# Kernel tuning notes

Hardware: AMD Instinct MI355X
Metric: run time of the kernel (lower is better)

## Reference

```python
import jax, jax.numpy as jnp
import numpy as np


def _mlp(x, W1, b1, W2, b2, W3, b3):
    # _F: three Linear layers, each followed by ReLU (including the last one)
    x = jax.nn.relu(x @ W1 + b1)
    x = jax.nn.relu(x @ W2 + b2)
    return jax.nn.relu(x @ W3 + b3)


def setup_inputs() -> dict:
    key = jax.random.key(0)
    ks = jax.random.split(key, 11)
    B, L, E, H, O = 2, 4096, 1024, 2048, 3  # batch pinned to 2 by view((2,-1,1))
    std = jnp.float32(0.02)  # small init keeps exp(fa.fb^T) finite in fp32
    z = lambda n: jnp.zeros((n,), jnp.float32)
    return {
        "x1": jax.random.normal(ks[0], (B, L, E), jnp.float32),
        "x2": jax.random.normal(ks[1], (B, L, E), jnp.float32),
        # attend.f = _F(E, H, H)
        "fW1": jax.random.normal(ks[2], (E, H), jnp.float32) * std, "fb1": z(H),
        "fW2": jax.random.normal(ks[3], (H, H), jnp.float32) * std, "fb2": z(H),
        "fW3": jax.random.normal(ks[4], (H, H), jnp.float32) * std, "fb3": z(H),
        # compare.g = _F(E, H, H)
        "gW1": jax.random.normal(ks[5], (E, H), jnp.float32) * std, "gb1": z(H),
        "gW2": jax.random.normal(ks[6], (H, H), jnp.float32) * std, "gb2": z(H),
        "gW3": jax.random.normal(ks[7], (H, H), jnp.float32) * std, "gb3": z(H),
        # aggregate.h = _F(2H, H, O)
        "hW1": jax.random.normal(ks[8], (2 * H, H), jnp.float32) * std, "hb1": z(H),
        "hW2": jax.random.normal(ks[9], (H, H), jnp.float32) * std, "hb2": z(H),
        "hW3": jax.random.normal(ks[10], (H, O), jnp.float32) * std, "hb3": z(O),
    }


def reference(x1, x2,
              fW1, fb1, fW2, fb2, fW3, fb3,
              gW1, gb1, gW2, gb2, gW3, gb3,
              hW1, hb1, hW2, hb2, hW3, hb3):
    # ---- Attend ----
    fa = _mlp(x1, fW1, fb1, fW2, fb2, fW3, fb3)  # (B, L, H)
    fb = _mlp(x2, fW1, fb1, fW2, fb2, fW3, fb3)  # (B, L, H)
    e = jnp.exp(jnp.einsum('bih,bjh->bij', fa, fb))  # (B, L, L), exp-then-normalize as in source
    # beta[b,i] = sum_j (e[b,i,j]/sum_j e[b,i,j]) * x2[b,j]
    beta = jnp.einsum('bij,bje->bie', e / jnp.sum(e, axis=2, keepdims=True), x2)
    # alpha[b,j] = sum_i (e[b,i,j]/sum_i e[b,i,j]) * x1[b,i]
    alpha = jnp.einsum('bij,bie->bje', e / jnp.sum(e, axis=1, keepdims=True), x1)
    # ---- Compare (note: concat along SEQUENCE dim=1, faithful to the source) ----
    v1 = _mlp(jnp.concatenate([x1, beta], axis=1), gW1, gb1, gW2, gb2, gW3, gb3)   # (B, 2L, H)
    v2 = _mlp(jnp.concatenate([x2, alpha], axis=1), gW1, gb1, gW2, gb2, gW3, gb3)  # (B, 2L, H)
    # ---- Aggregate ----
    agg = jnp.concatenate([jnp.sum(v1, axis=1), jnp.sum(v2, axis=1)], axis=1)  # (B, 2H)
    out = _mlp(agg, hW1, hb1, hW2, hb2, hW3, hb3)  # (B, O)
    return out
```

## Files before the change

kernel.cpp:

```cpp
#include <hip/hip_runtime.h>
#include <hip/hip_bf16.h>
#include <cstdint>
#include <cstddef>

typedef unsigned short ushort_t;
typedef __attribute__((ext_vector_type(8))) __bf16 bf16x8;
typedef __attribute__((ext_vector_type(4))) float f32x4;
typedef __attribute__((ext_vector_type(4))) unsigned short us4;

__device__ __forceinline__ unsigned short f2bf(float f) {
    union { __hip_bfloat16 h; unsigned short u; } v;
    v.h = __float2bfloat16(f);
    return v.u;
}
__device__ __forceinline__ float bf2f(unsigned short u) {
    union { unsigned int i; float f; } v;
    v.i = ((unsigned int)u) << 16;
    return v.f;
}

__device__ __forceinline__ void gload16(const void* g, void* l) {
    __builtin_amdgcn_global_load_lds((const __attribute__((address_space(1))) void*)g,
                                     (__attribute__((address_space(3))) void*)l,
                                     16, 0, 0);
}

#define BARRIER() asm volatile("s_barrier" ::: "memory")

template<int EPI>
__global__ __launch_bounds__(512) void gemm256(
        const ushort_t* __restrict__ A, const ushort_t* __restrict__ Bt,
        ushort_t* __restrict__ C, int M, int N, int K,
        const float* __restrict__ epi_vec, float* __restrict__ rowp)
{
    __shared__ __align__(16) ushort_t lds[65536];
    __shared__ float red[2][256];
    __shared__ float rowred[4][256];

    const int nN = N >> 8;
    const int nwg = (int)gridDim.x;
    const int orig = (int)blockIdx.x;
    const int q = nwg >> 3, r = nwg & 7, xcd = orig & 7;
    const int wgid = (xcd < r ? xcd * (q + 1) : r * (q + 1) + (xcd - r) * q) + (orig >> 3);
    const int mb = wgid / nN, nb = wgid % nN;

    const int t = (int)threadIdx.x;
    const int lane = t & 63;
    const int wave = t >> 6;
    const int wm = wave >> 2;
    const int wn = wave & 3;
    const int fr = lane & 15;
    const int fk = lane >> 4;

    const int NT = K >> 6;

    const int l8 = lane >> 3;
    const int lcc = ((lane & 7) ^ (l8 & 7)) * 8;
    const ushort_t* gA = A + (size_t)(mb * 256 + wave * 8 + l8) * (size_t)K + lcc;
    const ushort_t* gB = Bt + (size_t)(nb * 256 + wave * 8 + l8) * (size_t)K + lcc;

    auto stage1 = [&](int op, int dd, int h, int j, int T2) {
        const ushort_t* g = (op ? gB : gA) + (size_t)(h * 128 + j * 64) * (size_t)K + T2 * 64;
        ushort_t* l = lds + ((op * 2 + dd) * 2 + h) * 8192 + j * 4096 + wave * 512;
        gload16(g, l);
    };
    auto stageAB8 = [&](int dd, int T2) {
        stage1(0, dd, 0, 0, T2); stage1(0, dd, 0, 1, T2);
        stage1(0, dd, 1, 0, T2); stage1(0, dd, 1, 1, T2);
        stage1(1, dd, 0, 0, T2); stage1(1, dd, 0, 1, T2);
        stage1(1, dd, 1, 0, T2); stage1(1, dd, 1, 1, T2);
    };

    const int chunk0 = ((fk) ^ (fr & 7)) * 8;
    const int chunk1 = ((4 + fk) ^ (fr & 7)) * 8;

    auto loadA4 = [&](int dd, int kh, int qm, bf16x8* dst) {
        const ushort_t* base = lds + ((0 * 2 + dd) * 2 + wm) * 8192;
        const int ck = kh ? chunk1 : chunk0;
#pragma unroll
        for (int mi = 0; mi < 4; ++mi)
            dst[mi] = *(const bf16x8*)(base + (qm * 64 + mi * 16 + fr) * 64 + ck);
    };
    auto loadB4 = [&](int dd, int kh, bf16x8* dst) {
        const ushort_t* base = lds + ((1 * 2 + dd) * 2 + (wn >> 1)) * 8192;
        const int ck = kh ? chunk1 : chunk0;
#pragma unroll
        for (int ni = 0; ni < 4; ++ni)
            dst[ni] = *(const bf16x8*)(base + ((wn & 1) * 64 + ni * 16 + fr) * 64 + ck);
    };

    f32x4 acc[8][4];
#pragma unroll
    for (int i = 0; i < 8; ++i)
#pragma unroll
        for (int j = 0; j < 4; ++j) acc[i][j] = f32x4{0.f, 0.f, 0.f, 0.f};

#define MM(QM, AV, BV) do {                                                      \
    _Pragma("unroll") for (int mi = 0; mi < 4; ++mi)                             \
    _Pragma("unroll") for (int ni = 0; ni < 4; ++ni)                             \
        acc[(QM) * 4 + mi][ni] = __builtin_amdgcn_mfma_f32_16x16x32_bf16(        \
            AV[mi], BV[ni], acc[(QM) * 4 + mi][ni], 0, 0, 0);                    \
} while (0)

#define TILE_SYNC() do {                                                         \
    __builtin_amdgcn_sched_barrier(0);                                           \
    asm volatile("s_waitcnt lgkmcnt(0) vmcnt(0)" ::: "memory");                  \
    __builtin_amdgcn_sched_barrier(0);                                           \
    BARRIER();                                                                   \
} while (0)

    stageAB8(0, 0);
    asm volatile("s_waitcnt vmcnt(0)" ::: "memory");
    BARRIER();

    for (int T = 0; T < NT; ++T) {
        const int d = T & 1;
        bf16x8 a0[4], a1[4], a2[4], a3[4], b0[4], b1[4];
        loadB4(d, 0, b0);
        loadA4(d, 0, 0, a0);
        if (T + 1 < NT) stageAB8(d ^ 1, T + 1);
        loadA4(d, 0, 1, a1);
        MM(0, a0, b0);
        loadB4(d, 1, b1);
        loadA4(d, 1, 0, a2);
        MM(1, a1, b0);
        loadA4(d, 1, 1, a3);
        MM(0, a2, b1);
        MM(1, a3, b1);
        TILE_SYNC();
    }

#undef MM
#undef TILE_SYNC

    if (EPI == 0) {
#pragma unroll
        for (int mi8 = 0; mi8 < 8; ++mi8) {
            const int row0 = mb * 256 + wm * 128 + (mi8 >> 2) * 64 + (mi8 & 3) * 16 + fk * 4;
#pragma unroll
            for (int ni = 0; ni < 4; ++ni) {
                const int col = nb * 256 + wn * 64 + ni * 16 + fr;
                const float bias = epi_vec[col];
                f32x4 v = acc[mi8][ni];
#pragma unroll
                for (int j = 0; j < 4; ++j)
                    C[(size_t)(row0 + j) * N + col] = f2bf(fmaxf(v[j] + bias, 0.f));
            }
        }
    } else if (EPI == 1) {
        float rsum[8][4];
#pragma unroll
        for (int mi8 = 0; mi8 < 8; ++mi8) {
            const int row0 = mb * 256 + wm * 128 + (mi8 >> 2) * 64 + (mi8 & 3) * 16 + fk * 4;
#pragma unroll
            for (int j = 0; j < 4; ++j) rsum[mi8][j] = 0.f;
#pragma unroll
            for (int ni = 0; ni < 4; ++ni) {
                const int col = nb * 256 + wn * 64 + ni * 16 + fr;
                f32x4 v = acc[mi8][ni];
#pragma unroll
                for (int j = 0; j < 4; ++j) {
                    float x = __expf(v[j]);
                    C[(size_t)(row0 + j) * N + col] = f2bf(x);
                    rsum[mi8][j] += x;
                }
            }
        }
#pragma unroll
        for (int mi8 = 0; mi8 < 8; ++mi8)
#pragma unroll
            for (int j = 0; j < 4; ++j) {
                float s = rsum[mi8][j];
                s += __shfl_xor(s, 1); s += __shfl_xor(s, 2);
                s += __shfl_xor(s, 4); s += __shfl_xor(s, 8);
                rsum[mi8][j] = s;
            }
        if (fr == 0) {
#pragma unroll
            for (int mi8 = 0; mi8 < 8; ++mi8)
#pragma unroll
                for (int j = 0; j < 4; ++j)
                    rowred[wn][wm * 128 + (mi8 >> 2) * 64 + (mi8 & 3) * 16 + fk * 4 + j] = rsum[mi8][j];
        }
        BARRIER();
        if (t < 256)
            rowp[(size_t)nb * M + mb * 256 + t] =
                rowred[0][t] + rowred[1][t] + rowred[2][t] + rowred[3][t];
    } else {
        float cs[4] = {0.f, 0.f, 0.f, 0.f};
#pragma unroll
        for (int ni = 0; ni < 4; ++ni) {
            const int col = nb * 256 + wn * 64 + ni * 16 + fr;
            const float bias = epi_vec[col];
#pragma unroll
            for (int mi8 = 0; mi8 < 8; ++mi8) {
                f32x4 v = acc[mi8][ni];
#pragma unroll
                for (int j = 0; j < 4; ++j) cs[ni] += fmaxf(v[j] + bias, 0.f);
            }
        }
#pragma unroll
        for (int ni = 0; ni < 4; ++ni) {
            float s = cs[ni];
            s += __shfl_down(s, 32);
            s += __shfl_down(s, 16);
            cs[ni] = s;
        }
        if (fk == 0) {
#pragma unroll
            for (int ni = 0; ni < 4; ++ni) red[wm][wn * 64 + ni * 16 + fr] = cs[ni];
        }
        BARRIER();
        if (t < 256) {
            float* colpart = (float*)C;
            colpart[(size_t)mb * N + nb * 256 + t] = red[0][t] + red[1][t];
        }
    }
    asm volatile("s_waitcnt vmcnt(0)" ::: "memory");
}

template<int EPI>
__global__ __launch_bounds__(256) void gemm_bt(
        const ushort_t* __restrict__ A, const ushort_t* __restrict__ Bt,
        ushort_t* __restrict__ C, int M, int N, int K,
        const float* __restrict__ epi_vec)
{
    __shared__ __align__(16) ushort_t As[128 * 32];
    __shared__ __align__(16) ushort_t Bs[128 * 32];

    const int nN = N >> 7;
    const int nwg = (int)gridDim.x;
    const int orig = (int)blockIdx.x;
    const int q = nwg >> 3, r = nwg & 7, xcd = orig & 7;
    const int wgid = (xcd < r ? xcd * (q + 1) : r * (q + 1) + (xcd - r) * q) + (orig >> 3);
    const int mb = wgid / nN, nb = wgid % nN;

    const int t = (int)threadIdx.x;
    const int lane = t & 63;
    const int wave = t >> 6;
    const int wrow = (wave >> 1) << 6;
    const int wcol = (wave & 1) << 6;
    const int fr = lane & 15;
    const int fk = lane >> 4;

    int aoffe[4], boffe[4];
#pragma unroll
    for (int i = 0; i < 4; ++i) {
        int ra = wrow + i * 16 + fr;
        aoffe[i] = ra * 32 + (((fk ^ (ra >> 1)) & 3) << 3);
        int rb = wcol + i * 16 + fr;
        boffe[i] = rb * 32 + (((fk ^ (rb >> 1)) & 3) << 3);
    }

    const int srow = t >> 2;
    const int sslot = (t & 3) ^ ((srow >> 1) & 3);
    const ushort_t* ga = A + (size_t)(mb * 128 + srow) * K + sslot * 8;
    const ushort_t* gb = Bt + (size_t)(nb * 128 + srow) * K + sslot * 8;
    const size_t rowskip = (size_t)64 * K;
    ushort_t* lA0 = As + wave * 512;
    ushort_t* lA1 = As + 2048 + wave * 512;
    ushort_t* lB0 = Bs + wave * 512;
    ushort_t* lB1 = Bs + 2048 + wave * 512;

    f32x4 acc[4][4] = {};

    const int kiters = K >> 5;
    for (int kt = 0; kt < kiters; ++kt) {
        gload16(ga, lA0);
        gload16(ga + rowskip, lA1);
        gload16(gb, lB0);
        gload16(gb + rowskip, lB1);
        __syncthreads();
        bf16x8 af[4], bvv[4];
#pragma unroll
        for (int i = 0; i < 4; ++i) af[i] = *(const bf16x8*)(As + aoffe[i]);
#pragma unroll
        for (int i = 0; i < 4; ++i) bvv[i] = *(const bf16x8*)(Bs + boffe[i]);
#pragma unroll
        for (int mi = 0; mi < 4; ++mi)
#pragma unroll
            for (int ni = 0; ni < 4; ++ni)
                acc[mi][ni] = __builtin_amdgcn_mfma_f32_16x16x32_bf16(af[mi], bvv[ni], acc[mi][ni], 0, 0, 0);
        __syncthreads();
        ga += 32; gb += 32;
    }

#pragma unroll
    for (int mi = 0; mi < 4; ++mi) {
        const int row0 = mb * 128 + wrow + mi * 16 + fk * 4;
#pragma unroll
        for (int ni = 0; ni < 4; ++ni) {
            const int col = nb * 128 + wcol + ni * 16 + fr;
            float bias = (EPI == 0) ? epi_vec[col] : 0.f;
            f32x4 v = acc[mi][ni];
#pragma unroll
            for (int j = 0; j < 4; ++j) {
                int row = row0 + j;
                float x = v[j];
                if (EPI == 0)      x = fmaxf(x + bias, 0.f);
                else if (EPI == 1) x = __expf(x);
                else               x = x * epi_vec[row];
                C[(size_t)row * N + col] = f2bf(x);
            }
        }
    }
}

__global__ __launch_bounds__(256) void convert_x_k(const float* __restrict__ in,
                                                   ushort_t* __restrict__ out)
{
    size_t i = ((size_t)blockIdx.x * 256 + threadIdx.x) * 4;
    float4 v = *(const float4*)(in + i);
    us4 o;
    o[0] = f2bf(v.x); o[1] = f2bf(v.y); o[2] = f2bf(v.z); o[3] = f2bf(v.w);
    *(us4*)(out + i) = o;
}

__global__ void transpose_bf16_k(const ushort_t* __restrict__ in, ushort_t* __restrict__ out,
                                 int R, int C)
{
    __shared__ ushort_t tile[32][33];
    size_t bo = (size_t)blockIdx.z * R * C;
    const ushort_t* pin = in + bo;
    ushort_t* pout = out + bo;
    int c0 = blockIdx.x << 5, r0 = blockIdx.y << 5;
    int tx = threadIdx.x, ty = threadIdx.y;
#pragma unroll
    for (int i = 0; i < 4; ++i)
        tile[ty + i * 8][tx] = pin[(size_t)(r0 + ty + i * 8) * C + c0 + tx];
    __syncthreads();
#pragma unroll
    for (int i = 0; i < 4; ++i)
        pout[(size_t)(c0 + ty + i * 8) * R + r0 + tx] = tile[tx][ty + i * 8];
}

__global__ void wt_transpose_k(const float* __restrict__ in, ushort_t* __restrict__ out,
                               int R, int C)
{
    __shared__ ushort_t tile[32][33];
    int c0 = blockIdx.x << 5, r0 = blockIdx.y << 5;
    int tx = threadIdx.x, ty = threadIdx.y;
#pragma unroll
    for (int i = 0; i < 4; ++i)
        tile[ty + i * 8][tx] = f2bf(in[(size_t)(r0 + ty + i * 8) * C + c0 + tx]);
    __syncthreads();
#pragma unroll
    for (int i = 0; i < 4; ++i)
        out[(size_t)(c0 + ty + i * 8) * R + r0 + tx] = tile[tx][ty + i * 8];
}

__global__ __launch_bounds__(256) void rowrecip_k(const float* __restrict__ rowp,
                                                  float* __restrict__ out, int Mrows)
{
    int idx = blockIdx.x * 256 + threadIdx.x;
    float s = 0.f;
#pragma unroll
    for (int i = 0; i < 16; ++i) s += rowp[(size_t)i * Mrows + idx];
    out[idx] = 1.0f / s;
}

__global__ __launch_bounds__(256) void agg_reduce_k(const float* __restrict__ part,
                                                    float* __restrict__ agg)
{
    int idx = blockIdx.x * 256 + threadIdx.x;
    int g = idx >> 11, col = idx & 2047;
    int half = g >> 1, b = g & 1;
    const float* p = part + (size_t)half * 64 * 2048;
    float s = 0.f;
    for (int rr = 0; rr < 16; ++rr)
        s += p[(size_t)(b * 16 + rr) * 2048 + col] +
             p[(size_t)(32 + b * 16 + rr) * 2048 + col];
    agg[b * 4096 + half * 2048 + col] = s;
}

__global__ __launch_bounds__(256) void h_part_k(const float* __restrict__ act,
                                                const float* __restrict__ W,
                                                float* __restrict__ part, int Kdim)
{
    int j = blockIdx.x * 256 + threadIdx.x;
    int kc = blockIdx.y;
    float a0 = 0.f, a1 = 0.f;
    int k0 = kc * 16;
#pragma unroll
    for (int i = 0; i < 16; ++i) {
        int k = k0 + i;
        float w = W[(size_t)k * 2048 + j];
        a0 += act[k] * w;
        a1 += act[Kdim + k] * w;
    }
    part[(size_t)(kc * 2 + 0) * 2048 + j] = a0;
    part[(size_t)(kc * 2 + 1) * 2048 + j] = a1;
}

__global__ __launch_bounds__(256) void h_reduce_mid_k(const float* __restrict__ part,
                                                      float* __restrict__ part2)
{
    int idx = blockIdx.x * 256 + threadIdx.x;
    int g2 = idx >> 12;
    int rrow = (idx >> 11) & 1, j = idx & 2047;
    float s = 0.f;
#pragma unroll
    for (int i = 0; i < 16; ++i)
        s += part[(size_t)(((g2 * 16 + i) * 2) + rrow) * 2048 + j];
    part2[(size_t)(g2 * 2 + rrow) * 2048 + j] = s;
}

__global__ __launch_bounds__(256) void h_reduce_k(const float* __restrict__ part2,
                                                  const float* __restrict__ bias,
                                                  float* __restrict__ out, int nkc)
{
    int idx = blockIdx.x * 256 + threadIdx.x;
    int rrow = idx >> 11, j = idx & 2047;
    float s = 0.f;
    for (int kc = 0; kc < nkc; ++kc) s += part2[(size_t)(kc * 2 + rrow) * 2048 + j];
    s += bias[j];
    out[rrow * 2048 + j] = fmaxf(s, 0.f);
}

__global__ __launch_bounds__(256) void h3_k(const float* __restrict__ a2,
                                            const float* __restrict__ W,
                                            const float* __restrict__ b3,
                                            float* __restrict__ out)
{
    __shared__ float red[6][256];
    int t = threadIdx.x;
    float acc[6] = {0, 0, 0, 0, 0, 0};
    for (int k = t; k < 2048; k += 256) {
        float x0 = a2[k], x1 = a2[2048 + k];
#pragma unroll
        for (int c = 0; c < 3; ++c) {
            float w = W[k * 3 + c];
            acc[c] += x0 * w;
            acc[3 + c] += x1 * w;
        }
    }
#pragma unroll
    for (int c = 0; c < 6; ++c) red[c][t] = acc[c];
    __syncthreads();
    if (t < 6) {
        float s = 0.f;
        for (int i = 0; i < 256; ++i) s += red[t][i];
        s += b3[t < 3 ? t : t - 3];
        out[t] = fmaxf(s, 0.f);
    }
}

__global__ void diag_k(float* __restrict__ out, unsigned long long wsmb)
{
    if (threadIdx.x < 6) out[threadIdx.x] = 10000.0f + (float)wsmb;
}

constexpr size_t MB = 1024ull * 1024;
constexpr size_t OFF_W1T  = 0;
constexpr size_t OFF_W2T  = OFF_W1T  + 2048ull * 1024 * 2;
constexpr size_t OFF_W3T  = OFF_W2T  + 2048ull * 2048 * 2;
constexpr size_t OFF_XBF  = OFF_W3T  + 2048ull * 2048 * 2;
constexpr size_t OFF_R1   = OFF_XBF  + 16384ull * 1024 * 2;
constexpr size_t OFF_R2   = OFF_R1   + 64 * MB;
constexpr size_t OFF_BETA = OFF_R2   + 64 * MB;
constexpr size_t OFF_ALPHA= OFF_BETA + 2ull * 4096 * 1024 * 2;
constexpr size_t OFF_PART = OFF_ALPHA+ 2ull * 4096 * 1024 * 2;
constexpr size_t OFF_RS   = OFF_PART + 2ull * 128 * 2048 * 4;
constexpr size_t OFF_CS   = OFF_RS   + 4096 * 4;
constexpr size_t OFF_AGG  = OFF_CS   + 4096 * 4;
constexpr size_t OFF_ROWP = OFF_AGG  + 8192 * 4;
constexpr size_t OFF_END  = OFF_ROWP + 16ull * 4096 * 4;

extern "C" void kernel_launch(void* const* d_in, const int* in_sizes, int n_in,
                              void* d_out, int out_size, void* d_ws, size_t ws_size,
                              hipStream_t stream)
{
    const float* x1  = (const float*)d_in[0];
    const float* x2  = (const float*)d_in[1];
    const float* fW1 = (const float*)d_in[2];  const float* fb1 = (const float*)d_in[3];
    const float* fW2 = (const float*)d_in[4];  const float* fb2 = (const float*)d_in[5];
    const float* fW3 = (const float*)d_in[6];  const float* fb3 = (const float*)d_in[7];
    const float* gW1 = (const float*)d_in[8];  const float* gb1 = (const float*)d_in[9];
    const float* gW2 = (const float*)d_in[10]; const float* gb2 = (const float*)d_in[11];
    const float* gW3 = (const float*)d_in[12]; const float* gb3 = (const float*)d_in[13];
    const float* hW1 = (const float*)d_in[14]; const float* hb1 = (const float*)d_in[15];
    const float* hW2 = (const float*)d_in[16]; const float* hb2 = (const float*)d_in[17];
    const float* hW3 = (const float*)d_in[18]; const float* hb3 = (const float*)d_in[19];

    float* out = (float*)d_out;

    if (ws_size < OFF_END) {
        diag_k<<<1, 64, 0, stream>>>(out, (unsigned long long)(ws_size >> 20));
        return;
    }

    char* ws = (char*)d_ws;
    ushort_t* W1T  = (ushort_t*)(ws + OFF_W1T);
    ushort_t* W2T  = (ushort_t*)(ws + OFF_W2T);
    ushort_t* W3T  = (ushort_t*)(ws + OFF_W3T);
    ushort_t* XBF  = (ushort_t*)(ws + OFF_XBF);
    ushort_t* R1   = (ushort_t*)(ws + OFF_R1);
    ushort_t* R2   = (ushort_t*)(ws + OFF_R2);
    ushort_t* BETA = (ushort_t*)(ws + OFF_BETA);
    ushort_t* ALPHA= (ushort_t*)(ws + OFF_ALPHA);
    float* PART  = (float*)(ws + OFF_PART);
    float* RS    = (float*)(ws + OFF_RS);
    float* CS    = (float*)(ws + OFF_CS);
    float* AGG   = (float*)(ws + OFF_AGG);
    float* ROWP  = (float*)(ws + OFF_ROWP);

    ushort_t* PING = R2;
    ushort_t* PONG = R2 + 16777216;
    ushort_t* E    = R2;
    ushort_t* X1T  = R2 + 16777216;
    ushort_t* X2T  = R2 + 25165824;
    float* PARTH = (float*)(ws + OFF_R2);
    float* PART2 = (float*)(ws + OFF_R2 + 4 * MB);
    float* A1    = (float*)(ws + OFF_R2 + 6 * MB);
    float* A2    = (float*)(ws + OFF_R2 + 6 * MB + 16384);

    dim3 tb(32, 8);

    convert_x_k<<<8192, 256, 0, stream>>>(x1, XBF);
    convert_x_k<<<8192, 256, 0, stream>>>(x2, XBF + 8192ull * 1024);

    wt_transpose_k<<<dim3(64, 32), tb, 0, stream>>>(fW1, W1T, 1024, 2048);
    wt_transpose_k<<<dim3(64, 64), tb, 0, stream>>>(fW2, W2T, 2048, 2048);
    wt_transpose_k<<<dim3(64, 64), tb, 0, stream>>>(fW3, W3T, 2048, 2048);

    for (int c = 0; c < 2; ++c) {
        const ushort_t* src = XBF + (size_t)c * 8192 * 1024;
        ushort_t* dst = R1 + (size_t)c * 8192 * 2048;
        gemm256<0><<<256, 512, 0, stream>>>(src, W1T, PING, 8192, 2048, 1024, fb1, nullptr);
        gemm256<0><<<256, 512, 0, stream>>>(PING, W2T, PONG, 8192, 2048, 2048, fb2, nullptr);
        gemm256<0><<<256, 512, 0, stream>>>(PONG, W3T, dst, 8192, 2048, 2048, fb3, nullptr);
    }

    transpose_bf16_k<<<dim3(32, 128, 2), tb, 0, stream>>>(XBF, X1T, 4096, 1024);
    transpose_bf16_k<<<dim3(32, 128, 2), tb, 0, stream>>>(XBF + 8192ull * 1024, X2T, 4096, 1024);

    for (int b = 0; b < 2; ++b) {
        const ushort_t* fa  = R1 + (size_t)b * 4096 * 2048;
        const ushort_t* fbp = R1 + (size_t)(8192 + b * 4096) * 2048;
        gemm256<1><<<256, 512, 0, stream>>>(fa, fbp, E, 4096, 4096, 2048, nullptr, ROWP);
        rowrecip_k<<<16, 256, 0, stream>>>(ROWP, RS, 4096);
        gemm_bt<2><<<256, 256, 0, stream>>>(E, X2T + (size_t)b * 1024 * 4096,
                                            BETA + (size_t)b * 4096 * 1024,
                                            4096, 1024, 4096, RS);
        gemm256<1><<<256, 512, 0, stream>>>(fbp, fa, E, 4096, 4096, 2048, nullptr, ROWP);
        rowrecip_k<<<16, 256, 0, stream>>>(ROWP, CS, 4096);
        gemm_bt<2><<<256, 256, 0, stream>>>(E, X1T + (size_t)b * 1024 * 4096,
                                            ALPHA + (size_t)b * 4096 * 1024,
                                            4096, 1024, 4096, CS);
    }

    wt_transpose_k<<<dim3(64, 32), tb, 0, stream>>>(gW1, W1T, 1024, 2048);
    wt_transpose_k<<<dim3(64, 64), tb, 0, stream>>>(gW2, W2T, 2048, 2048);
    wt_transpose_k<<<dim3(64, 64), tb, 0, stream>>>(gW3, W3T, 2048, 2048);

    for (int c = 0; c < 2; ++c) {
        const ushort_t* xsrc = XBF + (size_t)c * 8192 * 1024;
        const ushort_t* asrc = (c == 0) ? BETA : ALPHA;
        gemm256<0><<<256, 512, 0, stream>>>(xsrc, W1T, R1, 8192, 2048, 1024, gb1, nullptr);
        gemm256<0><<<256, 512, 0, stream>>>(asrc, W1T, R1 + 8192ull * 2048, 8192, 2048, 1024, gb1, nullptr);
        gemm256<0><<<512, 512, 0, stream>>>(R1, W2T, R2, 16384, 2048, 2048, gb2, nullptr);
        gemm256<3><<<512, 512, 0, stream>>>(R2, W3T,
                                            (ushort_t*)(PART + (size_t)c * 64 * 2048),
                                            16384, 2048, 2048, gb3, nullptr);
    }
    agg_reduce_k<<<32, 256, 0, stream>>>(PART, AGG);

    h_part_k<<<dim3(8, 256), 256, 0, stream>>>(AGG, hW1, PARTH, 4096);
    h_reduce_mid_k<<<256, 256, 0, stream>>>(PARTH, PART2);
    h_reduce_k<<<16, 256, 0, stream>>>(PART2, hb1, A1, 16);
    h_part_k<<<dim3(8, 128), 256, 0, stream>>>(A1, hW2, PARTH, 2048);
    h_reduce_mid_k<<<128, 256, 0, stream>>>(PARTH, PART2);
    h_reduce_k<<<16, 256, 0, stream>>>(PART2, hb2, A2, 8);
    h3_k<<<1, 256, 0, stream>>>(A2, hW3, hb3, out);
}
```

Measured before the change: 1.614 ms.

## Compute score matrix once, derive column sums and transpose in place

The second exp-score GEMM (fb·fa^T) is removed. The first GEMM's epilogue now also accumulates per-column partial sums of exp, and an in-place 32x32 tiled transpose of E produces the matrix the alpha GEMM needs. This trades a 4096x4096x2048 GEMM for a memory-bound transpose of a 32MB bf16 matrix and a little extra epilogue reduction work.

```diff
diff --git a/kernel.cpp b/kernel.cpp
--- a/kernel.cpp
+++ b/kernel.cpp
@@ -31,7 +31,8 @@
 __global__ __launch_bounds__(512) void gemm256(
         const ushort_t* __restrict__ A, const ushort_t* __restrict__ Bt,
         ushort_t* __restrict__ C, int M, int N, int K,
-        const float* __restrict__ epi_vec, float* __restrict__ rowp)
+        const float* __restrict__ epi_vec, float* __restrict__ rowp,
+        float* __restrict__ colp)
 {
     __shared__ __align__(16) ushort_t lds[65536];
     __shared__ float red[2][256];
@@ -149,6 +150,7 @@
         }
     } else if (EPI == 1) {
         float rsum[8][4];
+        float csum[4] = {0.f, 0.f, 0.f, 0.f};
 #pragma unroll
         for (int mi8 = 0; mi8 < 8; ++mi8) {
             const int row0 = mb * 256 + wm * 128 + (mi8 >> 2) * 64 + (mi8 & 3) * 16 + fk * 4;
@@ -163,6 +165,7 @@
                     float x = __expf(v[j]);
                     C[(size_t)(row0 + j) * N + col] = f2bf(x);
                     rsum[mi8][j] += x;
+                    csum[ni] += x;
                 }
             }
         }
@@ -182,10 +185,23 @@
                 for (int j = 0; j < 4; ++j)
                     rowred[wn][wm * 128 + (mi8 >> 2) * 64 + (mi8 & 3) * 16 + fk * 4 + j] = rsum[mi8][j];
         }
+#pragma unroll
+        for (int ni = 0; ni < 4; ++ni) {
+            float s = csum[ni];
+            s += __shfl_down(s, 32);
+            s += __shfl_down(s, 16);
+            csum[ni] = s;
+        }
+        if (fk == 0) {
+#pragma unroll
+            for (int ni = 0; ni < 4; ++ni) red[wm][wn * 64 + ni * 16 + fr] = csum[ni];
+        }
         BARRIER();
-        if (t < 256)
+        if (t < 256) {
             rowp[(size_t)nb * M + mb * 256 + t] =
                 rowred[0][t] + rowred[1][t] + rowred[2][t] + rowred[3][t];
+            colp[(size_t)mb * N + nb * 256 + t] = red[0][t] + red[1][t];
+        }
     } else {
         float cs[4] = {0.f, 0.f, 0.f, 0.f};
 #pragma unroll
@@ -334,6 +350,32 @@
         pout[(size_t)(c0 + ty + i * 8) * R + r0 + tx] = tile[tx][ty + i * 8];
 }
 
+__global__ void transpose_inplace_k(ushort_t* __restrict__ Mx)
+{
+    int bi = blockIdx.y, bj = blockIdx.x;
+    if (bi > bj) return;
+    __shared__ ushort_t ta[32][33], tb[32][33];
+    int r0 = bi << 5, c0 = bj << 5;
+    int tx = threadIdx.x, ty = threadIdx.y;
+#pragma unroll
+    for (int i = 0; i < 4; ++i)
+        ta[ty + i * 8][tx] = Mx[(size_t)(r0 + ty + i * 8) * 4096 + c0 + tx];
+    if (bi < bj) {
+#pragma unroll
+        for (int i = 0; i < 4; ++i)
+            tb[ty + i * 8][tx] = Mx[(size_t)(c0 + ty + i * 8) * 4096 + r0 + tx];
+    }
+    __syncthreads();
+#pragma unroll
+    for (int i = 0; i < 4; ++i)
+        Mx[(size_t)(c0 + ty + i * 8) * 4096 + r0 + tx] = ta[tx][ty + i * 8];
+    if (bi < bj) {
+#pragma unroll
+        for (int i = 0; i < 4; ++i)
+            Mx[(size_t)(r0 + ty + i * 8) * 4096 + c0 + tx] = tb[tx][ty + i * 8];
+    }
+}
+
 __global__ void wt_transpose_k(const float* __restrict__ in, ushort_t* __restrict__ out,
                                int R, int C)
 {
@@ -349,13 +391,13 @@
         out[(size_t)(c0 + ty + i * 8) * R + r0 + tx] = tile[tx][ty + i * 8];
 }
 
-__global__ __launch_bounds__(256) void rowrecip_k(const float* __restrict__ rowp,
+__global__ __launch_bounds__(256) void rowrecip_k(const float* __restrict__ p,
                                                   float* __restrict__ out, int Mrows)
 {
     int idx = blockIdx.x * 256 + threadIdx.x;
     float s = 0.f;
 #pragma unroll
-    for (int i = 0; i < 16; ++i) s += rowp[(size_t)i * Mrows + idx];
+    for (int i = 0; i < 16; ++i) s += p[(size_t)i * Mrows + idx];
     out[idx] = 1.0f / s;
 }
 
@@ -464,7 +506,8 @@
 constexpr size_t OFF_CS   = OFF_RS   + 4096 * 4;
 constexpr size_t OFF_AGG  = OFF_CS   + 4096 * 4;
 constexpr size_t OFF_ROWP = OFF_AGG  + 8192 * 4;
-constexpr size_t OFF_END  = OFF_ROWP + 16ull * 4096 * 4;
+constexpr size_t OFF_COLP = OFF_ROWP + 16ull * 4096 * 4;
+constexpr size_t OFF_END  = OFF_COLP + 16ull * 4096 * 4;
 
 extern "C" void kernel_launch(void* const* d_in, const int* in_sizes, int n_in,
                               void* d_out, int out_size, void* d_ws, size_t ws_size,
@@ -503,6 +546,7 @@
     float* CS    = (float*)(ws + OFF_CS);
     float* AGG   = (float*)(ws + OFF_AGG);
     float* ROWP  = (float*)(ws + OFF_ROWP);
+    float* COLP  = (float*)(ws + OFF_COLP);
 
     ushort_t* PING = R2;
     ushort_t* PONG = R2 + 16777216;
@@ -526,9 +570,9 @@
     for (int c = 0; c < 2; ++c) {
         const ushort_t* src = XBF + (size_t)c * 8192 * 1024;
         ushort_t* dst = R1 + (size_t)c * 8192 * 2048;
-        gemm256<0><<<256, 512, 0, stream>>>(src, W1T, PING, 8192, 2048, 1024, fb1, nullptr);
-        gemm256<0><<<256, 512, 0, stream>>>(PING, W2T, PONG, 8192, 2048, 2048, fb2, nullptr);
-        gemm256<0><<<256, 512, 0, stream>>>(PONG, W3T, dst, 8192, 2048, 2048, fb3, nullptr);
+        gemm256<0><<<256, 512, 0, stream>>>(src, W1T, PING, 8192, 2048, 1024, fb1, nullptr, nullptr);
+        gemm256<0><<<256, 512, 0, stream>>>(PING, W2T, PONG, 8192, 2048, 2048, fb2, nullptr, nullptr);
+        gemm256<0><<<256, 512, 0, stream>>>(PONG, W3T, dst, 8192, 2048, 2048, fb3, nullptr, nullptr);
     }
 
     transpose_bf16_k<<<dim3(32, 128, 2), tb, 0, stream>>>(XBF, X1T, 4096, 1024);
@@ -537,13 +581,13 @@
     for (int b = 0; b < 2; ++b) {
         const ushort_t* fa  = R1 + (size_t)b * 4096 * 2048;
         const ushort_t* fbp = R1 + (size_t)(8192 + b * 4096) * 2048;
-        gemm256<1><<<256, 512, 0, stream>>>(fa, fbp, E, 4096, 4096, 2048, nullptr, ROWP);
+        gemm256<1><<<256, 512, 0, stream>>>(fa, fbp, E, 4096, 4096, 2048, nullptr, ROWP, COLP);
         rowrecip_k<<<16, 256, 0, stream>>>(ROWP, RS, 4096);
+        rowrecip_k<<<16, 256, 0, stream>>>(COLP, CS, 4096);
         gemm_bt<2><<<256, 256, 0, stream>>>(E, X2T + (size_t)b * 1024 * 4096,
                                             BETA + (size_t)b * 4096 * 1024,
                                             4096, 1024, 4096, RS);
-        gemm256<1><<<256, 512, 0, stream>>>(fbp, fa, E, 4096, 4096, 2048, nullptr, ROWP);
-        rowrecip_k<<<16, 256, 0, stream>>>(ROWP, CS, 4096);
+        transpose_inplace_k<<<dim3(128, 128), tb, 0, stream>>>(E);
         gemm_bt<2><<<256, 256, 0, stream>>>(E, X1T + (size_t)b * 1024 * 4096,
                                             ALPHA + (size_t)b * 4096 * 1024,
                                             4096, 1024, 4096, CS);
@@ -556,12 +600,12 @@
     for (int c = 0; c < 2; ++c) {
         const ushort_t* xsrc = XBF + (size_t)c * 8192 * 1024;
         const ushort_t* asrc = (c == 0) ? BETA : ALPHA;
-        gemm256<0><<<256, 512, 0, stream>>>(xsrc, W1T, R1, 8192, 2048, 1024, gb1, nullptr);
-        gemm256<0><<<256, 512, 0, stream>>>(asrc, W1T, R1 + 8192ull * 2048, 8192, 2048, 1024, gb1, nullptr);
-        gemm256<0><<<512, 512, 0, stream>>>(R1, W2T, R2, 16384, 2048, 2048, gb2, nullptr);
+        gemm256<0><<<256, 512, 0, stream>>>(xsrc, W1T, R1, 8192, 2048, 1024, gb1, nullptr, nullptr);
+        gemm256<0><<<256, 512, 0, stream>>>(asrc, W1T, R1 + 8192ull * 2048, 8192, 2048, 1024, gb1, nullptr, nullptr);
+        gemm256<0><<<512, 512, 0, stream>>>(R1, W2T, R2, 16384, 2048, 2048, gb2, nullptr, nullptr);
         gemm256<3><<<512, 512, 0, stream>>>(R2, W3T,
                                             (ushort_t*)(PART + (size_t)c * 64 * 2048),
-                                            16384, 2048, 2048, gb3, nullptr);
+                                            16384, 2048, 2048, gb3, nullptr, nullptr);
     }
     agg_reduce_k<<<32, 256, 0, stream>>>(PART, AGG);
 
```

New measurement: 1.523 ms. 1.06x faster.
